# Kernel tuning notes

Hardware: AMD Instinct MI355X
Metric: run time of the kernel (lower is better)

The kernel has to match this reference:

```python
import jax, jax.numpy as jnp
import numpy as np

V_MIN, V_MAX, ATOMS, GAMMA = -40.0, 80.0, 51, 0.9
BATCH = 524288


def setup_inputs() -> dict:
    key = jax.random.key(0)
    k1, k2, k3 = jax.random.split(key, 3)
    p = jax.random.uniform(k1, (BATCH, ATOMS), dtype=jnp.float32)
    prob_next = p / jnp.sum(p, axis=-1, keepdims=True)  # valid categorical dist
    r = jax.random.normal(k2, (BATCH, 1), dtype=jnp.float32) * 10.0
    done = (jax.random.uniform(k3, (BATCH, 1)) < 0.1).astype(jnp.float32)
    return {"prob_next": prob_next, "r": r, "done": done}


def reference(prob_next, r, done):
    # C51 categorical projection (DistributionalDQN.singleBatch target computation)
    B, A = prob_next.shape
    delta = (V_MAX - V_MIN) / float(A - 1)
    support = jnp.linspace(V_MIN, V_MAX, A, dtype=prob_next.dtype)  # [A]
    atom_next = jnpp_clip = jnp.clip(r + GAMMA * (1.0 - done) * support[None, :], V_MIN, V_MAX)  # [B,A]
    b = (atom_next - V_MIN) / delta
    l = jnp.floor(b)
    u = jnp.ceil(b)
    d_m_l = (u + (l == u).astype(b.dtype) - b) * prob_next
    d_m_u = (b - l) * prob_next
    # vectorized per-row index_add_: flatten rows with offsets and do one scatter-add
    offs = (jnp.arange(B, dtype=jnp.int32) * A)[:, None]  # [B,1]
    li = offs + l.astype(jnp.int32)
    ui = offs + u.astype(jnp.int32)
    flat = jnp.zeros(B * A, dtype=prob_next.dtype)
    flat = flat.at[li.ravel()].add(d_m_l.ravel())
    flat = flat.at[ui.ravel()].add(d_m_u.ravel())
    return flat.reshape(B, A)
```

## Files before the change

### kernel.cpp

```cpp
#include <hip/hip_runtime.h>


#define ATOMS 51
#define RPB   64
#define THREADS 64
#define TILE_FLOATS (RPB * ATOMS)
#define TILE_VECS   (TILE_FLOATS / 4)
#define VEC_ITERS   ((TILE_VECS + THREADS - 1) / THREADS)

__global__ __launch_bounds__(THREADS) void c51_project(
    const float* __restrict__ prob,
    const float* __restrict__ rin,
    const float* __restrict__ done,
    float* __restrict__ out,
    int nrows)
{
    __shared__ __align__(16) float s_buf[TILE_FLOATS];
    const int t = threadIdx.x;
    const long long row0 = (long long)blockIdx.x * RPB;
    const int rows_here = (int)min((long long)RPB, (long long)nrows - row0);
    const bool full = (rows_here == RPB);

    if (full) {
        const float4* gsrc = reinterpret_cast<const float4*>(prob + (size_t)row0 * ATOMS);
        float4* sv = reinterpret_cast<float4*>(s_buf);
        #pragma unroll
        for (int i = 0; i < VEC_ITERS; ++i) {
            const int v = i * THREADS + t;
            if (v < TILE_VECS) sv[v] = gsrc[v];
        }
    } else {
        const int n_e = rows_here * ATOMS;
        const float* gsrc = prob + (size_t)row0 * ATOMS;
        for (int e = t; e < n_e; e += THREADS) s_buf[e] = gsrc[e];
    }
    __syncthreads();

    if (t < rows_here) {
        const float rr = rin[row0 + t];
        const float c  = 0.9f * (1.0f - done[row0 + t]);
        const float base = fmaf(-16.66666667f, c, (rr + 40.0f) * (1.0f / 2.4f));
        const int ib = t * ATOMS;

        float p[ATOMS];
        #pragma unroll
        for (int j = 0; j < ATOMS; ++j) p[j] = s_buf[ib + j];

        #pragma unroll
        for (int i = 0; i < ATOMS; ++i) s_buf[ib + i] = 0.0f;

        int   cur   = (int)floorf(fminf(fmaxf(base, 0.0f), 50.0f));
        float vcur  = 0.0f, vnext = 0.0f;
        #pragma unroll
        for (int j = 0; j < ATOMS; ++j) {
            float b = fmaf(c, (float)j, base);
            b = fminf(fmaxf(b, 0.0f), 50.0f);
            const float lf = floorf(b);
            const float f  = b - lf;
            const int  li  = (int)lf;
            while (li > cur) {
                s_buf[ib + cur] = vcur;
                vcur = vnext; vnext = 0.0f; ++cur;
            }
            vcur  = fmaf(1.0f - f, p[j], vcur);
            vnext = fmaf(f,        p[j], vnext);
        }
        s_buf[ib + cur] = vcur;
        if (cur < ATOMS - 1) s_buf[ib + cur + 1] = vnext;
    }
    __syncthreads();

    if (full) {
        float4* dst = reinterpret_cast<float4*>(out + (size_t)row0 * ATOMS);
        const float4* sv = reinterpret_cast<const float4*>(s_buf);
        #pragma unroll
        for (int i = 0; i < VEC_ITERS; ++i) {
            const int v = i * THREADS + t;
            if (v < TILE_VECS) dst[v] = sv[v];
        }
    } else {
        const int n_e = rows_here * ATOMS;
        float* dst = out + (size_t)row0 * ATOMS;
        for (int e = t; e < n_e; e += THREADS) dst[e] = s_buf[e];
    }
}

extern "C" void kernel_launch(void* const* d_in, const int* in_sizes, int n_in,
                              void* d_out, int out_size, void* d_ws, size_t ws_size,
                              hipStream_t stream) {
    const float* prob = (const float*)d_in[0];
    const float* r    = (const float*)d_in[1];
    const float* done = (const float*)d_in[2];
    float* outp = (float*)d_out;
    const int B = in_sizes[1];
    const int grid = (B + RPB - 1) / RPB;
    c51_project<<<dim3(grid), dim3(THREADS), 0, stream>>>(prob, r, done, outp, B);
}
```

Baseline: 49.15 us.

## Make kernel persistent with double-buffered async global-to-LDS tile staging

Replaces the one-tile-per-block launch with a grid-capped persistent loop over 64-row tiles. Each iteration prefetches the next tile of probabilities straight into a second LDS buffer with global_load_lds, plus the next r and done values, while the current tile is projected and written back. A manual s_waitcnt vmcnt stands in for block barriers, which relies on each block being a single wavefront. The aim is to hide load latency and cut launch and block-scheduling overhead. The cost is a doubled LDS footprint and fewer resident waves, which may limit memory-level parallelism.

```diff
diff --git a/kernel.cpp b/kernel.cpp
--- a/kernel.cpp
+++ b/kernel.cpp
@@ -1,4 +1,5 @@
 #include <hip/hip_runtime.h>
+#include <stdint.h>
 
 
 #define ATOMS 51
@@ -6,7 +7,54 @@
 #define THREADS 64
 #define TILE_FLOATS (RPB * ATOMS)
 #define TILE_VECS   (TILE_FLOATS / 4)
-#define VEC_ITERS   ((TILE_VECS + THREADS - 1) / THREADS)
+#define STAGE_ITERS ((TILE_VECS + THREADS - 1) / THREADS)
+#define GRID_MAX 1536
+
+typedef const __attribute__((address_space(1))) void gvoid_t;
+typedef __attribute__((address_space(3))) void lvoid_t;
+
+__device__ __forceinline__ void stage_tile(const float* gbase, float* lbase, int t) {
+    #pragma unroll
+    for (int i = 0; i < STAGE_ITERS; ++i) {
+        const int v = i * THREADS + t;
+        if (v < TILE_VECS) {
+            __builtin_amdgcn_global_load_lds((gvoid_t*)(gbase + (size_t)v * 4),
+                                             (lvoid_t*)(lbase + i * THREADS * 4),
+                                             16, 0, 0);
+        }
+    }
+}
+
+__device__ __forceinline__ void compute_row(float* sb, int t, float rr, float dn) {
+    const float c = 0.9f * (1.0f - dn);
+    const float base = fmaf(-16.66666667f, c, (rr + 40.0f) * (1.0f / 2.4f));
+    const int ib = t * ATOMS;
+
+    float p[ATOMS];
+    #pragma unroll
+    for (int j = 0; j < ATOMS; ++j) p[j] = sb[ib + j];
+    #pragma unroll
+    for (int j = 0; j < ATOMS; ++j) sb[ib + j] = 0.0f;
+
+    int   cur  = (int)floorf(fminf(fmaxf(base, 0.0f), 50.0f));
+    float vcur = 0.0f, vnext = 0.0f;
+    #pragma unroll
+    for (int j = 0; j < ATOMS; ++j) {
+        float b = fmaf(c, (float)j, base);
+        b = fminf(fmaxf(b, 0.0f), 50.0f);
+        const float lf = floorf(b);
+        const float f  = b - lf;
+        const int  li  = (int)lf;
+        while (li > cur) {
+            sb[ib + cur] = vcur;
+            vcur = vnext; vnext = 0.0f; ++cur;
+        }
+        vcur  = fmaf(1.0f - f, p[j], vcur);
+        vnext = fmaf(f,        p[j], vnext);
+    }
+    sb[ib + cur] = vcur;
+    if (cur < ATOMS - 1) sb[ib + cur + 1] = vnext;
+}
 
 __global__ __launch_bounds__(THREADS) void c51_project(
     const float* __restrict__ prob,
@@ -15,71 +63,57 @@
     float* __restrict__ out,
     int nrows)
 {
-    __shared__ __align__(16) float s_buf[TILE_FLOATS];
+    __shared__ __align__(16) float s_buf[2 * TILE_FLOATS];
     const int t = threadIdx.x;
-    const long long row0 = (long long)blockIdx.x * RPB;
-    const int rows_here = (int)min((long long)RPB, (long long)nrows - row0);
-    const bool full = (rows_here == RPB);
+    const int G = gridDim.x;
+    const int ntiles = nrows / RPB;
+    const int tail_rows = nrows - ntiles * RPB;
 
-    if (full) {
-        const float4* gsrc = reinterpret_cast<const float4*>(prob + (size_t)row0 * ATOMS);
-        float4* sv = reinterpret_cast<float4*>(s_buf);
-        #pragma unroll
-        for (int i = 0; i < VEC_ITERS; ++i) {
-            const int v = i * THREADS + t;
-            if (v < TILE_VECS) sv[v] = gsrc[v];
+    int tk = blockIdx.x;
+    if (tk < ntiles) {
+        stage_tile(prob + (size_t)tk * TILE_FLOATS, s_buf, t);
+        float rv = rin[(size_t)tk * RPB + t];
+        float dv = done[(size_t)tk * RPB + t];
+        int buf = 0;
+
+        for (; tk < ntiles; tk += G) {
+            const int nxt = tk + G;
+            float rnx = 0.0f, dnx = 0.0f;
+            if (nxt < ntiles) {
+                stage_tile(prob + (size_t)nxt * TILE_FLOATS,
+                           s_buf + (buf ^ 1) * TILE_FLOATS, t);
+                rnx = rin[(size_t)nxt * RPB + t];
+                dnx = done[(size_t)nxt * RPB + t];
+                asm volatile("s_waitcnt vmcnt(15)" ::: "memory");
+            } else {
+                asm volatile("s_waitcnt vmcnt(0)" ::: "memory");
+            }
+            __builtin_amdgcn_sched_barrier(0);
+
+            float* sb = s_buf + buf * TILE_FLOATS;
+            compute_row(sb, t, rv, dv);
+
+            float4* dst = reinterpret_cast<float4*>(out + (size_t)tk * TILE_FLOATS);
+            const float4* sv = reinterpret_cast<const float4*>(sb);
+            #pragma unroll
+            for (int i = 0; i < STAGE_ITERS; ++i) {
+                const int v = i * THREADS + t;
+                if (v < TILE_VECS) dst[v] = sv[v];
+            }
+
+            rv = rnx; dv = dnx;
+            buf ^= 1;
         }
-    } else {
-        const int n_e = rows_here * ATOMS;
+    }
+
+    if (tail_rows > 0 && blockIdx.x == 0) {
+        const long long row0 = (long long)ntiles * RPB;
+        const int n_e = tail_rows * ATOMS;
         const float* gsrc = prob + (size_t)row0 * ATOMS;
         for (int e = t; e < n_e; e += THREADS) s_buf[e] = gsrc[e];
-    }
-    __syncthreads();
-
-    if (t < rows_here) {
-        const float rr = rin[row0 + t];
-        const float c  = 0.9f * (1.0f - done[row0 + t]);
-        const float base = fmaf(-16.66666667f, c, (rr + 40.0f) * (1.0f / 2.4f));
-        const int ib = t * ATOMS;
-
-        float p[ATOMS];
-        #pragma unroll
-        for (int j = 0; j < ATOMS; ++j) p[j] = s_buf[ib + j];
-
-        #pragma unroll
-        for (int i = 0; i < ATOMS; ++i) s_buf[ib + i] = 0.0f;
-
-        int   cur   = (int)floorf(fminf(fmaxf(base, 0.0f), 50.0f));
-        float vcur  = 0.0f, vnext = 0.0f;
-        #pragma unroll
-        for (int j = 0; j < ATOMS; ++j) {
-            float b = fmaf(c, (float)j, base);
-            b = fminf(fmaxf(b, 0.0f), 50.0f);
-            const float lf = floorf(b);
-            const float f  = b - lf;
-            const int  li  = (int)lf;
-            while (li > cur) {
-                s_buf[ib + cur] = vcur;
-                vcur = vnext; vnext = 0.0f; ++cur;
-            }
-            vcur  = fmaf(1.0f - f, p[j], vcur);
-            vnext = fmaf(f,        p[j], vnext);
-        }
-        s_buf[ib + cur] = vcur;
-        if (cur < ATOMS - 1) s_buf[ib + cur + 1] = vnext;
-    }
-    __syncthreads();
-
-    if (full) {
-        float4* dst = reinterpret_cast<float4*>(out + (size_t)row0 * ATOMS);
-        const float4* sv = reinterpret_cast<const float4*>(s_buf);
-        #pragma unroll
-        for (int i = 0; i < VEC_ITERS; ++i) {
-            const int v = i * THREADS + t;
-            if (v < TILE_VECS) dst[v] = sv[v];
-        }
-    } else {
-        const int n_e = rows_here * ATOMS;
+        __syncthreads();
+        if (t < tail_rows) compute_row(s_buf, t, rin[row0 + t], done[row0 + t]);
+        __syncthreads();
         float* dst = out + (size_t)row0 * ATOMS;
         for (int e = t; e < n_e; e += THREADS) dst[e] = s_buf[e];
     }
@@ -93,6 +127,8 @@
     const float* done = (const float*)d_in[2];
     float* outp = (float*)d_out;
     const int B = in_sizes[1];
-    const int grid = (B + RPB - 1) / RPB;
+    const int ntiles = B / RPB;
+    int grid = ntiles < GRID_MAX ? ntiles : GRID_MAX;
+    if (grid < 1) grid = 1;
     c51_project<<<dim3(grid), dim3(THREADS), 0, stream>>>(prob, r, done, outp, B);
 }
```

After: 47.39 us. 3.6% less time.
